# Kernel tuning notes

Measured on AMD Instinct MI355X. Metric: run time of the kernel, lower is better.

The kernel has to match this reference:

```python
import jax, jax.numpy as jnp
import numpy as np

B, P, ENC, DEC, ATT, EMB, V, T = 128, 196, 2048, 512, 512, 512, 10000, 30


def setup_inputs() -> dict:
    key = jax.random.key(0)
    ks = jax.random.split(key, 16)

    def lin(k, o, i, s=0.02):
        k1, k2 = jax.random.split(k)
        return (jax.random.normal(k1, (o, i), jnp.float32) * s,
                jax.random.normal(k2, (o,), jnp.float32) * s)

    enc_out = jax.random.normal(ks[0], (B, P, ENC), jnp.float32)
    enc_caps = jax.random.randint(ks[1], (B, T), 0, V)
    len_caps = jax.random.randint(ks[2], (B, 1), 2, T + 1)  # lengths in [2, T]

    W_enc_att, b_enc_att = lin(ks[3], ATT, ENC)
    W_dec_att, b_dec_att = lin(ks[4], ATT, DEC)
    W_att, b_att = lin(ks[5], 1, ATT)
    W_init_h, b_init_h = lin(ks[6], DEC, ENC)
    W_init_c, b_init_c = lin(ks[7], DEC, ENC)
    W_ih, b_ih = lin(ks[8], 4 * DEC, EMB + ENC)
    W_hh, b_hh = lin(ks[9], 4 * DEC, DEC)
    W_fbeta, b_fbeta = lin(ks[10], ENC, DEC)
    emb = jax.random.uniform(ks[11], (V, EMB), jnp.float32, -0.1, 0.1)
    W_fc = jax.random.uniform(ks[12], (V, DEC), jnp.float32, -0.1, 0.1)
    b_fc = jnp.zeros((V,), jnp.float32)

    return dict(enc_out=enc_out, enc_caps=enc_caps, len_caps=len_caps, emb=emb,
                W_enc_att=W_enc_att, b_enc_att=b_enc_att,
                W_dec_att=W_dec_att, b_dec_att=b_dec_att,
                W_att=W_att, b_att=b_att,
                W_init_h=W_init_h, b_init_h=b_init_h,
                W_init_c=W_init_c, b_init_c=b_init_c,
                W_ih=W_ih, b_ih=b_ih, W_hh=W_hh, b_hh=b_hh,
                W_fbeta=W_fbeta, b_fbeta=b_fbeta,
                W_fc=W_fc, b_fc=b_fc)


def _forward(enc_out, enc_caps, len_caps, emb,
             W_enc_att, b_enc_att, W_dec_att, b_dec_att, W_att, b_att,
             W_init_h, b_init_h, W_init_c, b_init_c,
             W_ih, b_ih, W_hh, b_hh, W_fbeta, b_fbeta, W_fc, b_fc):
    lens = len_caps[:, 0]
    order = jnp.argsort(-lens)  # sort descending by caption length
    lens = lens[order]
    caps = enc_caps[order]
    enc = enc_out[order]  # [B,P,ENC]
    len_dec = lens - 1
    Tm = caps.shape[1] - 1  # static upper bound on decode steps; masked per row

    embeds = emb[caps[:, :Tm]]  # [B,Tm,EMB]
    mu = enc.mean(axis=1)
    h = mu @ W_init_h.T + b_init_h
    c = mu @ W_init_c.T + b_init_c
    att_enc = enc @ W_enc_att.T + b_enc_att  # [B,P,ATT], invariant over t

    def step(carry, inp):
        h, c = carry
        t, emb_t = inp
        att_dec = h @ W_dec_att.T + b_dec_att  # [B,ATT]
        e = (jax.nn.relu(att_enc + att_dec[:, None, :]) @ W_att.T + b_att)[..., 0]  # [B,P]
        alpha = jax.nn.softmax(e, axis=1)
        weighted = jnp.einsum('bpd,bp->bd', enc, alpha)  # [B,ENC]
        gate = jax.nn.sigmoid(h @ W_fbeta.T + b_fbeta)
        x = jnp.concatenate([emb_t, weighted * gate], axis=1)  # [B,EMB+ENC]
        gates = x @ W_ih.T + b_ih + h @ W_hh.T + b_hh
        i, f, g, o = jnp.split(gates, 4, axis=1)  # torch LSTMCell gate order
        c_new = jax.nn.sigmoid(f) * c + jax.nn.sigmoid(i) * jnp.tanh(g)
        h_new = jax.nn.sigmoid(o) * jnp.tanh(c_new)
        preds = h_new @ W_fc.T + b_fc  # dropout is identity at eval
        m = (t < len_dec).astype(h.dtype)[:, None]  # shrinking-batch mask
        h = m * h_new + (1 - m) * h
        c = m * c_new + (1 - m) * c
        return (h, c), (preds * m, alpha * m)

    ts = jnp.arange(Tm)
    (_, _), (preds, alphas) = jax.lax.scan(step, (h, c), (ts, jnp.swapaxes(embeds, 0, 1)))
    predictions = jnp.swapaxes(preds, 0, 1)  # [B,Tm,V]
    alphas = jnp.swapaxes(alphas, 0, 1)      # [B,Tm,P]
    return caps, len_dec, predictions, alphas, order


def reference(enc_out, enc_caps, len_caps, emb,
              W_enc_att, b_enc_att, W_dec_att, b_dec_att, W_att, b_att,
              W_init_h, b_init_h, W_init_c, b_init_c,
              W_ih, b_ih, W_hh, b_hh, W_fbeta, b_fbeta, W_fc, b_fc):
    return _forward(enc_out, enc_caps, len_caps, emb,
                    W_enc_att, b_enc_att, W_dec_att, b_dec_att, W_att, b_att,
                    W_init_h, b_init_h, W_init_c, b_init_c,
                    W_ih, b_ih, W_hh, b_hh, W_fbeta, b_fbeta, W_fc, b_fc)
```

## Files before the change

### kernel.cpp

```cpp
#include <hip/hip_runtime.h>
#include <hip/hip_bf16.h>
#include <math.h>

#define NB   128
#define NP   196
#define DENC 2048
#define DDEC 512
#define NV   10000
#define NT   30
#define NTM  29

typedef __attribute__((ext_vector_type(8))) short short8;
typedef __attribute__((ext_vector_type(4))) float f32x4;

__device__ __forceinline__ float sigmoidf_(float x) { return 1.f / (1.f + __expf(-x)); }
__device__ __forceinline__ unsigned short f2bf(float x) {
    unsigned int u = __float_as_uint(x);
    u += 0x7fffu + ((u >> 16) & 1u);
    return (unsigned short)(u >> 16);
}
__device__ __forceinline__ float bf2f(unsigned short h) {
    return __uint_as_float(((unsigned int)h) << 16);
}

__global__ void sort_kernel(const int* __restrict__ len_caps,
                            const int* __restrict__ enc_caps,
                            float* __restrict__ out_caps,
                            float* __restrict__ out_lendec,
                            float* __restrict__ out_order,
                            int* __restrict__ order_ws,
                            int* __restrict__ nt_ws,
                            int* __restrict__ caps_ws) {
    __shared__ int lens[NB];
    int i = threadIdx.x;
    lens[i] = len_caps[i];
    __syncthreads();
    int li = lens[i];
    int r = 0;
    for (int j = 0; j < NB; ++j) {
        int lj = lens[j];
        if (lj > li || (lj == li && j < i)) r++;
    }
    order_ws[r]   = i;
    out_order[r]  = (float)i;
    out_lendec[r] = (float)(li - 1);
    for (int k = 0; k < NT; ++k) {
        int cv = enc_caps[i * NT + k];
        caps_ws[r * NT + k]  = cv;
        out_caps[r * NT + k] = (float)cv;
    }
    if (i < NTM) {
        int cnt = 0;
        for (int j = 0; j < NB; ++j) cnt += (lens[j] - 1 > i) ? 1 : 0;
        nt_ws[i] = cnt;
    }
}

__global__ void rowmap_kernel(const int* __restrict__ order, int* __restrict__ rowmap) {
    int m = blockIdx.x * 256 + threadIdx.x;
    rowmap[m] = order[m / NP] * NP + (m % NP);
}

__global__ void mu_kernel(const float* __restrict__ enc,
                          const int* __restrict__ order,
                          float* __restrict__ mu) {
    int b = blockIdx.x;
    int d = blockIdx.y * 256 + threadIdx.x;
    const float* eb = enc + (long)order[b] * NP * DENC;
    float s = 0.f;
    for (int p = 0; p < NP; ++p) s += eb[(long)p * DENC + d];
    mu[(long)b * DENC + d] = s * (1.f / (float)NP);
}

__global__ void fill_zero4(float4* __restrict__ p, int n4) {
    int i = blockIdx.x * 256 + threadIdx.x;
    if (i < n4) p[i] = make_float4(0.f, 0.f, 0.f, 0.f);
}

__global__ void conv_bf(const float* __restrict__ s, unsigned short* __restrict__ d, int n) {
    int i = blockIdx.x * 256 + threadIdx.x;
    if (i < n) d[i] = f2bf(s[i]);
}

__global__ void kconcat_ihh(const float* __restrict__ W_ih, const float* __restrict__ W_hh,
                            unsigned short* __restrict__ dst) {
    int n = blockIdx.y;
    int k = blockIdx.x * 256 + threadIdx.x;
    float v = (k < 2560) ? W_ih[(long)n * 2560 + k] : W_hh[(long)n * 512 + (k - 2560)];
    dst[(long)n * 3072 + k] = f2bf(v);
}

__global__ void bias_add2(const float* __restrict__ a, const float* __restrict__ b,
                          float* __restrict__ d, int n) {
    int i = blockIdx.x * 256 + threadIdx.x;
    if (i < n) d[i] = a[i] + b[i];
}

__global__ __launch_bounds__(256) void gemm_mfma(
    const float* __restrict__ A, long lda, const int* __restrict__ rowmap,
    const unsigned short* __restrict__ W, long ldw,
    const float* __restrict__ bias0, const float* __restrict__ bias1, int split,
    float* __restrict__ out0, long ld0, float* __restrict__ out1, long ld1,
    unsigned short* __restrict__ outbf,
    int act0, int act1, int M, int N, int K,
    const int* __restrict__ nt, int t, long zstride) {
    __shared__ __align__(16) unsigned short As[64 * 32];
    __shared__ __align__(16) unsigned short Bs[128 * 32];
    const int limit = nt ? nt[t] : M;

    int bx = blockIdx.x, by = blockIdx.y;
    if (!nt) {
        int nwg = gridDim.x * gridDim.y;
        int lin = by * gridDim.x + bx;
        int q = nwg >> 3, r = nwg & 7;
        int xcd = lin & 7, i = lin >> 3;
        int sw = (xcd < r ? xcd * (q + 1) : r * (q + 1) + (xcd - r) * q) + i;
        bx = sw % gridDim.x;
        by = sw / gridDim.x;
    }

    const int m0 = by * 64;
    if (m0 >= limit) return;
    const int n0 = bx * 128;
    const int tid = threadIdx.x;
    const int kz = blockIdx.z * K;

    const int arow = tid >> 2, ak = (tid & 3) * 8;
    const int brow = tid >> 1, bk = (tid & 1) * 16;
    long aRowG = m0 + arow;
    if (rowmap) aRowG = rowmap[aRowG];
    const float* aptr = A + aRowG * lda + ak + kz;
    const int gnw = n0 + brow;
    const bool wvalid = gnw < N;
    const unsigned short* wptr = W + (long)(wvalid ? gnw : 0) * ldw + bk + kz;

    if (blockIdx.z) out0 += (long)blockIdx.z * zstride;

    const int lane = tid & 63, wv = tid >> 6;
    const int wm = wv & 1, wn = wv >> 1;
    const int fcol = lane & 15, quad = lane >> 4;
    const unsigned short* aFp = As + ((wm * 32 + fcol) * 32 + quad * 8);
    const unsigned short* bFp = Bs + ((wn * 64 + fcol) * 32 + quad * 8);

    f32x4 acc[2][4];
#pragma unroll
    for (int i = 0; i < 2; ++i)
#pragma unroll
        for (int j = 0; j < 4; ++j) acc[i][j] = (f32x4){0.f, 0.f, 0.f, 0.f};

    for (int k0 = 0; k0 < K; k0 += 32) {
        float4 x0 = *(const float4*)(aptr);
        float4 x1 = *(const float4*)(aptr + 4);
        aptr += 32;
        int4 w0 = make_int4(0, 0, 0, 0), w1 = w0;
        if (wvalid) {
            w0 = *(const int4*)(wptr);
            w1 = *(const int4*)(wptr + 8);
        }
        wptr += 32;
        short8 ap;
        ap[0] = (short)f2bf(x0.x); ap[1] = (short)f2bf(x0.y);
        ap[2] = (short)f2bf(x0.z); ap[3] = (short)f2bf(x0.w);
        ap[4] = (short)f2bf(x1.x); ap[5] = (short)f2bf(x1.y);
        ap[6] = (short)f2bf(x1.z); ap[7] = (short)f2bf(x1.w);
        __syncthreads();
        *(short8*)(As + (arow * 32 + ak)) = ap;
        *(int4*)(Bs + (brow * 32 + bk)) = w0;
        *(int4*)(Bs + (brow * 32 + bk + 8)) = w1;
        __syncthreads();
        short8 a0 = *(const short8*)(aFp);
        short8 a1 = *(const short8*)(aFp + 512);
#pragma unroll
        for (int ns = 0; ns < 4; ++ns) {
            short8 bn = *(const short8*)(bFp + ns * 512);
            acc[0][ns] = __builtin_amdgcn_mfma_f32_16x16x32_bf16(a0, bn, acc[0][ns], 0, 0, 0);
            acc[1][ns] = __builtin_amdgcn_mfma_f32_16x16x32_bf16(a1, bn, acc[1][ns], 0, 0, 0);
        }
    }

#pragma unroll
    for (int ms = 0; ms < 2; ++ms) {
        int gmb = m0 + wm * 32 + ms * 16 + quad * 4;
#pragma unroll
        for (int ns = 0; ns < 4; ++ns) {
            int gn = n0 + wn * 64 + ns * 16 + fcol;
            if (gn >= N) continue;
            int seg = (gn >= split);
            float bv = seg ? (bias1 ? bias1[gn - split] : 0.f)
                           : (bias0 ? bias0[gn] : 0.f);
            int act = seg ? act1 : act0;
#pragma unroll
            for (int r = 0; r < 4; ++r) {
                int gm = gmb + r;
                if (gm >= limit) continue;
                float v = acc[ms][ns][r] + bv;
                if (act == 1) v = sigmoidf_(v);
                if (outbf) outbf[(long)gm * ld0 + gn] = f2bf(v);
                else if (!seg) out0[(long)gm * ld0 + gn] = v;
                else out1[(long)gm * ld1 + (gn - split)] = v;
            }
        }
    }
}

__global__ __launch_bounds__(256) void alpha_kernel(
    const unsigned short* __restrict__ att_enc,
    const float* __restrict__ adg,
    const float* __restrict__ W_att, const float* __restrict__ b_att,
    const float* __restrict__ emb, const int* __restrict__ caps,
    const float* __restrict__ h,
    const int* __restrict__ nt,
    float* __restrict__ al_g,
    float* __restrict__ out_alpha,
    float* __restrict__ xh, int t) {
    int b = blockIdx.x;
    if (b >= nt[t]) return;
    int tid = threadIdx.x, lane = tid & 63, wid = tid >> 6;
    __shared__ float es[NP];
    __shared__ float stats[2];

    const float* adp = adg + (long)b * 2560 + lane * 8;
    float4 ad0 = *(const float4*)(adp);
    float4 ad1 = *(const float4*)(adp + 4);
    const float* wap = W_att + lane * 8;
    float4 wa0 = *(const float4*)(wap);
    float4 wa1 = *(const float4*)(wap + 4);
    float ad[8] = {ad0.x, ad0.y, ad0.z, ad0.w, ad1.x, ad1.y, ad1.z, ad1.w};
    float wa[8] = {wa0.x, wa0.y, wa0.z, wa0.w, wa1.x, wa1.y, wa1.z, wa1.w};
    float batt = b_att[0];

    for (int p = wid; p < NP; p += 4) {
        const unsigned short* row = att_enc + ((long)b * NP + p) * 512 + lane * 8;
        int4 rv = *(const int4*)row;
        const unsigned short* us = (const unsigned short*)&rv;
        float s = 0.f;
#pragma unroll
        for (int j = 0; j < 8; ++j) {
            float v = bf2f(us[j]) + ad[j];
            v = v > 0.f ? v : 0.f;
            s += v * wa[j];
        }
#pragma unroll
        for (int o = 32; o; o >>= 1) s += __shfl_xor(s, o, 64);
        if (lane == 0) es[p] = s + batt;
    }
    __syncthreads();
    if (wid == 0) {
        float v[4], mx = -1e30f;
#pragma unroll
        for (int i = 0; i < 4; ++i) {
            int p = lane + 64 * i;
            v[i] = (p < NP) ? es[p] : -1e30f;
            mx = fmaxf(mx, v[i]);
        }
#pragma unroll
        for (int o = 32; o; o >>= 1) mx = fmaxf(mx, __shfl_xor(mx, o, 64));
        float s = 0.f;
#pragma unroll
        for (int i = 0; i < 4; ++i) {
            int p = lane + 64 * i;
            if (p < NP) s += __expf(v[i] - mx);
        }
#pragma unroll
        for (int o = 32; o; o >>= 1) s += __shfl_xor(s, o, 64);
        if (lane == 0) { stats[0] = mx; stats[1] = 1.f / s; }
    }
    __syncthreads();
    float mm = stats[0], inv = stats[1];
    if (tid < NP) {
        float a = __expf(es[tid] - mm) * inv;
        al_g[(long)b * NP + tid] = a;
        out_alpha[((long)b * NTM + t) * NP + tid] = a;
    }
    int cap = caps[b * NT + t];
    float2 ev = *(const float2*)(emb + (long)cap * 512 + tid * 2);
    *(float2*)(xh + (long)b * 3072 + tid * 2) = ev;
    float2 hv = *(const float2*)(h + (long)b * DDEC + tid * 2);
    *(float2*)(xh + (long)b * 3072 + 2560 + tid * 2) = hv;
}

__global__ __launch_bounds__(256) void wx_kernel(
    const float* __restrict__ al_g,
    const float* __restrict__ adg,
    const float* __restrict__ enc, const int* __restrict__ order,
    const int* __restrict__ nt,
    float* __restrict__ xh, int t) {
    int b = blockIdx.x;
    if (b >= nt[t]) return;
    int d = blockIdx.y * 256 + threadIdx.x;
    __shared__ float al[NP];
    if (threadIdx.x < NP) al[threadIdx.x] = al_g[(long)b * NP + threadIdx.x];
    __syncthreads();
    const float* eb = enc + ((long)order[b] * NP) * DENC + d;
    float acc = 0.f;
#pragma unroll 4
    for (int p = 0; p < NP; ++p) acc += al[p] * eb[(long)p * DENC];
    float gate = adg[(long)b * 2560 + 512 + d];
    xh[(long)b * 3072 + 512 + d] = acc * gate;
}

__global__ void lstm_kernel(const float* __restrict__ gp,
                            const float* __restrict__ bihh,
                            float* __restrict__ c,
                            float* __restrict__ h,
                            const int* __restrict__ nt, int t) {
    int b = blockIdx.y;
    if (b >= nt[t]) return;
    int d = blockIdx.x * 256 + threadIdx.x;
    const long S = (long)NB * 2048;
    const float* g = gp + ((long)b << 11);
    float ig = sigmoidf_(g[d]        + g[S + d]        + g[2*S + d]        + bihh[d]);
    float fg = sigmoidf_(g[512 + d]  + g[S + 512 + d]  + g[2*S + 512 + d]  + bihh[512 + d]);
    float gg = tanhf(    g[1024 + d] + g[S + 1024 + d] + g[2*S + 1024 + d] + bihh[1024 + d]);
    float og = sigmoidf_(g[1536 + d] + g[S + 1536 + d] + g[2*S + 1536 + d] + bihh[1536 + d]);
    long idx = (long)b * DDEC + d;
    float cn = fg * c[idx] + ig * gg;
    c[idx] = cn;
    h[idx] = og * tanhf(cn);
}

extern "C" void kernel_launch(void* const* d_in, const int* in_sizes, int n_in,
                              void* d_out, int out_size, void* d_ws, size_t ws_size,
                              hipStream_t stream) {
    const float* enc_out   = (const float*)d_in[0];
    const int*   enc_caps  = (const int*)d_in[1];
    const int*   len_caps  = (const int*)d_in[2];
    const float* emb       = (const float*)d_in[3];
    const float* W_enc_att = (const float*)d_in[4];
    const float* b_enc_att = (const float*)d_in[5];
    const float* W_dec_att = (const float*)d_in[6];
    const float* b_dec_att = (const float*)d_in[7];
    const float* W_att     = (const float*)d_in[8];
    const float* b_att     = (const float*)d_in[9];
    const float* W_init_h  = (const float*)d_in[10];
    const float* b_init_h  = (const float*)d_in[11];
    const float* W_init_c  = (const float*)d_in[12];
    const float* b_init_c  = (const float*)d_in[13];
    const float* W_ih      = (const float*)d_in[14];
    const float* b_ih      = (const float*)d_in[15];
    const float* W_hh      = (const float*)d_in[16];
    const float* b_hh      = (const float*)d_in[17];
    const float* W_fbeta   = (const float*)d_in[18];
    const float* b_fbeta   = (const float*)d_in[19];
    const float* W_fc      = (const float*)d_in[20];
    const float* b_fc      = (const float*)d_in[21];

    float* out        = (float*)d_out;
    float* out_caps   = out;
    float* out_lendec = out + 3840;
    float* out_pred   = out + 3968;
    float* out_alpha  = out + 3968 + 37120000;
    float* out_order  = out + 3968 + 37120000 + 727552;

    char*  wsb = (char*)d_ws;
    size_t off = 0;
    auto alloc = [&](size_t bytes) -> void* {
        void* p = wsb + off;
        off += (bytes + 255) & ~(size_t)255;
        return p;
    };
    int*   order_ws = (int*)alloc(NB * 4);
    int*   nt_ws    = (int*)alloc(NTM * 4);
    int*   caps_ws  = (int*)alloc(NB * NT * 4);
    int*   rowmap   = (int*)alloc((size_t)NB * NP * 4);
    float* mu       = (float*)alloc((size_t)NB * DENC * 4);
    float* h        = (float*)alloc((size_t)NB * DDEC * 4);
    float* c        = (float*)alloc((size_t)NB * DDEC * 4);
    float* adg      = (float*)alloc((size_t)NB * 2560 * 4);
    float* al_g     = (float*)alloc((size_t)NB * NP * 4);
    float* xh       = (float*)alloc((size_t)NB * 3072 * 4);
    float* gates    = (float*)alloc((size_t)3 * NB * 2048 * 4);
    unsigned short* att_enc_bf = (unsigned short*)alloc((size_t)NB * NP * 512 * 2);
    unsigned short* Wq_enc  = (unsigned short*)alloc((size_t)512 * 2048 * 2);
    unsigned short* Wq_init = (unsigned short*)alloc((size_t)1024 * 2048 * 2);
    unsigned short* Wq_adg  = (unsigned short*)alloc((size_t)2560 * 512 * 2);
    unsigned short* Wq_ihh  = (unsigned short*)alloc((size_t)2048 * 3072 * 2);
    unsigned short* Wq_fc   = (unsigned short*)alloc((size_t)NV * 512 * 2);
    float* bihh = (float*)alloc(2048 * 4);

    sort_kernel<<<1, NB, 0, stream>>>(len_caps, enc_caps, out_caps, out_lendec,
                                      out_order, order_ws, nt_ws, caps_ws);
    fill_zero4<<<36960, 256, 0, stream>>>((float4*)out_pred, 9461888);
    rowmap_kernel<<<98, 256, 0, stream>>>(order_ws, rowmap);
    mu_kernel<<<dim3(NB, DENC / 256), 256, 0, stream>>>(enc_out, order_ws, mu);

    conv_bf<<<(512 * 2048) / 256, 256, 0, stream>>>(W_enc_att, Wq_enc, 512 * 2048);
    conv_bf<<<(512 * 2048) / 256, 256, 0, stream>>>(W_init_h, Wq_init, 512 * 2048);
    conv_bf<<<(512 * 2048) / 256, 256, 0, stream>>>(W_init_c, Wq_init + (size_t)512 * 2048, 512 * 2048);
    conv_bf<<<(512 * 512) / 256, 256, 0, stream>>>(W_dec_att, Wq_adg, 512 * 512);
    conv_bf<<<(2048 * 512) / 256, 256, 0, stream>>>(W_fbeta, Wq_adg + (size_t)512 * 512, 2048 * 512);
    kconcat_ihh<<<dim3(12, 2048), 256, 0, stream>>>(W_ih, W_hh, Wq_ihh);
    conv_bf<<<(NV * 512) / 256, 256, 0, stream>>>(W_fc, Wq_fc, NV * 512);
    bias_add2<<<8, 256, 0, stream>>>(b_ih, b_hh, bihh, 2048);

    gemm_mfma<<<dim3(8, 2), 256, 0, stream>>>(
        mu, DENC, nullptr, Wq_init, DENC,
        b_init_h, b_init_c, 512,
        h, DDEC, c, DDEC, nullptr, 0, 0,
        NB, 1024, DENC, nullptr, 0, 0);

    gemm_mfma<<<dim3(4, 392), 256, 0, stream>>>(
        enc_out, DENC, rowmap, Wq_enc, DENC,
        b_enc_att, nullptr, 512,
        nullptr, 512, nullptr, 0, att_enc_bf, 0, 0,
        NB * NP, 512, DENC, nullptr, 0, 0);

    for (int t = 0; t < NTM; ++t) {
        gemm_mfma<<<dim3(20, 2), 256, 0, stream>>>(
            h, DDEC, nullptr, Wq_adg, DDEC,
            b_dec_att, b_fbeta, 512,
            adg, 2560, adg + 512, 2560, nullptr, 0, 1,
            NB, 2560, DDEC, nt_ws, t, 0);
        alpha_kernel<<<NB, 256, 0, stream>>>(
            att_enc_bf, adg, W_att, b_att, emb, caps_ws, h, nt_ws,
            al_g, out_alpha, xh, t);
        wx_kernel<<<dim3(NB, 8), 256, 0, stream>>>(
            al_g, adg, enc_out, order_ws, nt_ws, xh, t);
        gemm_mfma<<<dim3(16, 2, 3), 256, 0, stream>>>(
            xh, 3072, nullptr, Wq_ihh, 3072,
            nullptr, nullptr, 2048,
            gates, 2048, nullptr, 0, nullptr, 0, 0,
            NB, 2048, 1024, nt_ws, t, (long)NB * 2048);
        lstm_kernel<<<dim3(2, NB), 256, 0, stream>>>(gates, bihh, c, h, nt_ws, t);
        gemm_mfma<<<dim3(79, 2), 256, 0, stream>>>(
            h, DDEC, nullptr, Wq_fc, DDEC,
            b_fc, nullptr, NV,
            out_pred + (long)t * NV, (long)NTM * NV, nullptr, 0, nullptr, 0, 0,
            NB, NV, DDEC, nt_ws, t, 0);
    }
}
```

Before: 4.394 ms.

## Store decoder activations in bf16 and XOR-swizzle GEMM LDS tiles

The hidden state h and the concatenated LSTM input xh are now stored directly as bf16. A new abf flag lets the MFMA GEMM load bf16 A operands without converting from fp32, which halves activation traffic in the per-step GEMMs. The shared-memory A and B tiles now use an XOR swizzle on the 8-element chunk index to reduce LDS bank conflicts on the fragment reads. Numerics are essentially unchanged, since the GEMM already rounded A to bf16, but h now only exists in bf16 between steps.

```diff
diff --git a/kernel.cpp b/kernel.cpp
--- a/kernel.cpp
+++ b/kernel.cpp
@@ -103,7 +103,7 @@
     float* __restrict__ out0, long ld0, float* __restrict__ out1, long ld1,
     unsigned short* __restrict__ outbf,
     int act0, int act1, int M, int N, int K,
-    const int* __restrict__ nt, int t, long zstride) {
+    const int* __restrict__ nt, int t, long zstride, int abf) {
     __shared__ __align__(16) unsigned short As[64 * 32];
     __shared__ __align__(16) unsigned short Bs[128 * 32];
     const int limit = nt ? nt[t] : M;
@@ -125,22 +125,31 @@
     const int tid = threadIdx.x;
     const int kz = blockIdx.z * K;
 
-    const int arow = tid >> 2, ak = (tid & 3) * 8;
-    const int brow = tid >> 1, bk = (tid & 1) * 16;
+    const int arow = tid >> 2, akc = tid & 3;
+    const int aws = (akc ^ ((arow >> 1) & 3)) * 8;
+    const int brow = tid >> 1, bkc = (tid & 1) * 2;
+    const int bss = (brow >> 1) & 3;
+    const int bws0 = (bkc ^ bss) * 8;
+    const int bws1 = ((bkc + 1) ^ bss) * 8;
+
     long aRowG = m0 + arow;
     if (rowmap) aRowG = rowmap[aRowG];
-    const float* aptr = A + aRowG * lda + ak + kz;
+    const float* aptrf = nullptr;
+    const unsigned short* aptrh = nullptr;
+    if (abf) aptrh = (const unsigned short*)A + aRowG * lda + akc * 8 + kz;
+    else     aptrf = A + aRowG * lda + akc * 8 + kz;
     const int gnw = n0 + brow;
     const bool wvalid = gnw < N;
-    const unsigned short* wptr = W + (long)(wvalid ? gnw : 0) * ldw + bk + kz;
+    const unsigned short* wptr = W + (long)(wvalid ? gnw : 0) * ldw + bkc * 8 + kz;
 
     if (blockIdx.z) out0 += (long)blockIdx.z * zstride;
 
     const int lane = tid & 63, wv = tid >> 6;
     const int wm = wv & 1, wn = wv >> 1;
     const int fcol = lane & 15, quad = lane >> 4;
-    const unsigned short* aFp = As + ((wm * 32 + fcol) * 32 + quad * 8);
-    const unsigned short* bFp = Bs + ((wn * 64 + fcol) * 32 + quad * 8);
+    const int sx = (fcol >> 1) & 3;
+    const unsigned short* aFp = As + ((wm * 32 + fcol) * 32 + ((quad ^ sx) * 8));
+    const unsigned short* bFp = Bs + ((wn * 64 + fcol) * 32 + ((quad ^ sx) * 8));
 
     f32x4 acc[2][4];
 #pragma unroll
@@ -149,24 +158,29 @@
         for (int j = 0; j < 4; ++j) acc[i][j] = (f32x4){0.f, 0.f, 0.f, 0.f};
 
     for (int k0 = 0; k0 < K; k0 += 32) {
-        float4 x0 = *(const float4*)(aptr);
-        float4 x1 = *(const float4*)(aptr + 4);
-        aptr += 32;
+        short8 ap;
+        if (abf) {
+            ap = *(const short8*)(aptrh);
+            aptrh += 32;
+        } else {
+            float4 x0 = *(const float4*)(aptrf);
+            float4 x1 = *(const float4*)(aptrf + 4);
+            aptrf += 32;
+            ap[0] = (short)f2bf(x0.x); ap[1] = (short)f2bf(x0.y);
+            ap[2] = (short)f2bf(x0.z); ap[3] = (short)f2bf(x0.w);
+            ap[4] = (short)f2bf(x1.x); ap[5] = (short)f2bf(x1.y);
+            ap[6] = (short)f2bf(x1.z); ap[7] = (short)f2bf(x1.w);
+        }
         int4 w0 = make_int4(0, 0, 0, 0), w1 = w0;
         if (wvalid) {
             w0 = *(const int4*)(wptr);
             w1 = *(const int4*)(wptr + 8);
         }
         wptr += 32;
-        short8 ap;
-        ap[0] = (short)f2bf(x0.x); ap[1] = (short)f2bf(x0.y);
-        ap[2] = (short)f2bf(x0.z); ap[3] = (short)f2bf(x0.w);
-        ap[4] = (short)f2bf(x1.x); ap[5] = (short)f2bf(x1.y);
-        ap[6] = (short)f2bf(x1.z); ap[7] = (short)f2bf(x1.w);
         __syncthreads();
-        *(short8*)(As + (arow * 32 + ak)) = ap;
-        *(int4*)(Bs + (brow * 32 + bk)) = w0;
-        *(int4*)(Bs + (brow * 32 + bk + 8)) = w1;
+        *(short8*)(As + (arow * 32 + aws)) = ap;
+        *(int4*)(Bs + (brow * 32 + bws0)) = w0;
+        *(int4*)(Bs + (brow * 32 + bws1)) = w1;
         __syncthreads();
         short8 a0 = *(const short8*)(aFp);
         short8 a1 = *(const short8*)(aFp + 512);
@@ -195,7 +209,7 @@
                 if (gm >= limit) continue;
                 float v = acc[ms][ns][r] + bv;
                 if (act == 1) v = sigmoidf_(v);
-                if (outbf) outbf[(long)gm * ld0 + gn] = f2bf(v);
+                if (outbf && !seg) outbf[(long)gm * ld0 + gn] = f2bf(v);
                 else if (!seg) out0[(long)gm * ld0 + gn] = v;
                 else out1[(long)gm * ld1 + (gn - split)] = v;
             }
@@ -208,11 +222,11 @@
     const float* __restrict__ adg,
     const float* __restrict__ W_att, const float* __restrict__ b_att,
     const float* __restrict__ emb, const int* __restrict__ caps,
-    const float* __restrict__ h,
+    const unsigned short* __restrict__ h_bf,
     const int* __restrict__ nt,
     float* __restrict__ al_g,
     float* __restrict__ out_alpha,
-    float* __restrict__ xh, int t) {
+    unsigned short* __restrict__ xh, int t) {
     int b = blockIdx.x;
     if (b >= nt[t]) return;
     int tid = threadIdx.x, lane = tid & 63, wid = tid >> 6;
@@ -274,9 +288,10 @@
     }
     int cap = caps[b * NT + t];
     float2 ev = *(const float2*)(emb + (long)cap * 512 + tid * 2);
-    *(float2*)(xh + (long)b * 3072 + tid * 2) = ev;
-    float2 hv = *(const float2*)(h + (long)b * DDEC + tid * 2);
-    *(float2*)(xh + (long)b * 3072 + 2560 + tid * 2) = hv;
+    unsigned int pk = (unsigned int)f2bf(ev.x) | ((unsigned int)f2bf(ev.y) << 16);
+    *(unsigned int*)(xh + (long)b * 3072 + tid * 2) = pk;
+    unsigned int hv = *(const unsigned int*)(h_bf + (long)b * DDEC + tid * 2);
+    *(unsigned int*)(xh + (long)b * 3072 + 2560 + tid * 2) = hv;
 }
 
 __global__ __launch_bounds__(256) void wx_kernel(
@@ -284,7 +299,7 @@
     const float* __restrict__ adg,
     const float* __restrict__ enc, const int* __restrict__ order,
     const int* __restrict__ nt,
-    float* __restrict__ xh, int t) {
+    unsigned short* __restrict__ xh, int t) {
     int b = blockIdx.x;
     if (b >= nt[t]) return;
     int d = blockIdx.y * 256 + threadIdx.x;
@@ -296,13 +311,13 @@
 #pragma unroll 4
     for (int p = 0; p < NP; ++p) acc += al[p] * eb[(long)p * DENC];
     float gate = adg[(long)b * 2560 + 512 + d];
-    xh[(long)b * 3072 + 512 + d] = acc * gate;
+    xh[(long)b * 3072 + 512 + d] = f2bf(acc * gate);
 }
 
 __global__ void lstm_kernel(const float* __restrict__ gp,
                             const float* __restrict__ bihh,
                             float* __restrict__ c,
-                            float* __restrict__ h,
+                            unsigned short* __restrict__ h_bf,
                             const int* __restrict__ nt, int t) {
     int b = blockIdx.y;
     if (b >= nt[t]) return;
@@ -316,7 +331,7 @@
     long idx = (long)b * DDEC + d;
     float cn = fg * c[idx] + ig * gg;
     c[idx] = cn;
-    h[idx] = og * tanhf(cn);
+    h_bf[idx] = f2bf(og * tanhf(cn));
 }
 
 extern "C" void kernel_launch(void* const* d_in, const int* in_sizes, int n_in,
@@ -364,12 +379,12 @@
     int*   caps_ws  = (int*)alloc(NB * NT * 4);
     int*   rowmap   = (int*)alloc((size_t)NB * NP * 4);
     float* mu       = (float*)alloc((size_t)NB * DENC * 4);
-    float* h        = (float*)alloc((size_t)NB * DDEC * 4);
     float* c        = (float*)alloc((size_t)NB * DDEC * 4);
     float* adg      = (float*)alloc((size_t)NB * 2560 * 4);
     float* al_g     = (float*)alloc((size_t)NB * NP * 4);
-    float* xh       = (float*)alloc((size_t)NB * 3072 * 4);
     float* gates    = (float*)alloc((size_t)3 * NB * 2048 * 4);
+    unsigned short* h_bf = (unsigned short*)alloc((size_t)NB * DDEC * 2);
+    unsigned short* xh   = (unsigned short*)alloc((size_t)NB * 3072 * 2);
     unsigned short* att_enc_bf = (unsigned short*)alloc((size_t)NB * NP * 512 * 2);
     unsigned short* Wq_enc  = (unsigned short*)alloc((size_t)512 * 2048 * 2);
     unsigned short* Wq_init = (unsigned short*)alloc((size_t)1024 * 2048 * 2);
@@ -396,36 +411,36 @@
     gemm_mfma<<<dim3(8, 2), 256, 0, stream>>>(
         mu, DENC, nullptr, Wq_init, DENC,
         b_init_h, b_init_c, 512,
-        h, DDEC, c, DDEC, nullptr, 0, 0,
-        NB, 1024, DENC, nullptr, 0, 0);
+        nullptr, DDEC, c, DDEC, h_bf, 0, 0,
+        NB, 1024, DENC, nullptr, 0, 0, 0);
 
     gemm_mfma<<<dim3(4, 392), 256, 0, stream>>>(
         enc_out, DENC, rowmap, Wq_enc, DENC,
         b_enc_att, nullptr, 512,
         nullptr, 512, nullptr, 0, att_enc_bf, 0, 0,
-        NB * NP, 512, DENC, nullptr, 0, 0);
+        NB * NP, 512, DENC, nullptr, 0, 0, 0);
 
     for (int t = 0; t < NTM; ++t) {
         gemm_mfma<<<dim3(20, 2), 256, 0, stream>>>(
-            h, DDEC, nullptr, Wq_adg, DDEC,
+            (const float*)h_bf, DDEC, nullptr, Wq_adg, DDEC,
             b_dec_att, b_fbeta, 512,
             adg, 2560, adg + 512, 2560, nullptr, 0, 1,
-            NB, 2560, DDEC, nt_ws, t, 0);
+            NB, 2560, DDEC, nt_ws, t, 0, 1);
         alpha_kernel<<<NB, 256, 0, stream>>>(
-            att_enc_bf, adg, W_att, b_att, emb, caps_ws, h, nt_ws,
+            att_enc_bf, adg, W_att, b_att, emb, caps_ws, h_bf, nt_ws,
             al_g, out_alpha, xh, t);
         wx_kernel<<<dim3(NB, 8), 256, 0, stream>>>(
             al_g, adg, enc_out, order_ws, nt_ws, xh, t);
         gemm_mfma<<<dim3(16, 2, 3), 256, 0, stream>>>(
-            xh, 3072, nullptr, Wq_ihh, 3072,
+            (const float*)xh, 3072, nullptr, Wq_ihh, 3072,
             nullptr, nullptr, 2048,
             gates, 2048, nullptr, 0, nullptr, 0, 0,
-            NB, 2048, 1024, nt_ws, t, (long)NB * 2048);
-        lstm_kernel<<<dim3(2, NB), 256, 0, stream>>>(gates, bihh, c, h, nt_ws, t);
+            NB, 2048, 1024, nt_ws, t, (long)NB * 2048, 1);
+        lstm_kernel<<<dim3(2, NB), 256, 0, stream>>>(gates, bihh, c, h_bf, nt_ws, t);
         gemm_mfma<<<dim3(79, 2), 256, 0, stream>>>(
-            h, DDEC, nullptr, Wq_fc, DDEC,
+            (const float*)h_bf, DDEC, nullptr, Wq_fc, DDEC,
             b_fc, nullptr, NV,
             out_pred + (long)t * NV, (long)NTM * NV, nullptr, 0, nullptr, 0, 0,
-            NB, NV, DDEC, nt_ws, t, 0);
-    }
-}
+            NB, NV, DDEC, nt_ws, t, 0, 1);
+    }
+}
```

Result: faster. 4.086 ms (-7.0%).
